# Kernel tuning notes

Hardware: AMD Instinct MI355X
Metric: run time of the kernel (lower is better)

## Reference

```python
import jax, jax.numpy as jnp
import numpy as np

N_NODES = 100000
N_EDGES = 100000
NNZ = 3200000
D_IN, D_HID, N_CLS = 512, 16, 7
NEG_SLOPE = 0.2


def _segment_softmax(scores, seg, num_segments, sorted_seg):
    m = jax.ops.segment_max(scores, seg, num_segments=num_segments,
                            indices_are_sorted=sorted_seg)
    ex = jnp.exp(scores - m[seg])
    s = jax.ops.segment_sum(ex, seg, num_segments=num_segments,
                            indices_are_sorted=sorted_seg)
    return ex / (s[seg] + 1e-9)


def _hypergat_layer(X, W, a1, a2, node_idx, edge_idx):
    # X: [N, din] -> h: [N, dout]
    h = X @ W
    hv = h[node_idx]                                   # [nnz, dout] gather
    # phase 1: node -> hyperedge attention (softmax within each hyperedge)
    s1 = jax.nn.leaky_relu(hv @ a1, NEG_SLOPE)         # [nnz]
    alpha = _segment_softmax(s1, edge_idx, N_EDGES, True)
    e = jax.ops.segment_sum(alpha[:, None] * hv, edge_idx,
                            num_segments=N_EDGES, indices_are_sorted=True)
    # phase 2: hyperedge -> node attention (softmax over edges incident to node)
    ev = e[edge_idx]                                   # [nnz, dout] gather
    s2 = jax.nn.leaky_relu(jnp.concatenate([hv, ev], axis=-1) @ a2, NEG_SLOPE)
    beta = _segment_softmax(s2, node_idx, N_NODES, False)
    out = jax.ops.segment_sum(beta[:, None] * ev, node_idx,
                              num_segments=N_NODES)
    return out


def setup_inputs() -> dict:
    key = jax.random.key(0)
    ks = jax.random.split(key, 8)
    H = jax.random.normal(ks[0], (N_NODES, D_IN), dtype=jnp.float32)
    node_idx = jax.random.randint(ks[1], (NNZ,), 0, N_NODES)
    edge_idx = jnp.sort(jax.random.randint(ks[2], (NNZ,), 0, N_EDGES))
    g1 = 1.0 / np.sqrt(D_IN)
    g2 = 1.0 / np.sqrt(D_HID)
    W1 = jax.random.uniform(ks[3], (D_IN, D_HID), jnp.float32, -g1, g1)
    a1_1 = jax.random.uniform(ks[4], (D_HID,), jnp.float32, -g2, g2)
    a2_1 = jax.random.uniform(ks[5], (2 * D_HID,), jnp.float32, -g2, g2)
    W2 = jax.random.uniform(ks[6], (D_HID, N_CLS), jnp.float32, -g2, g2)
    k7, k8 = jax.random.split(ks[7])
    gc = 1.0 / np.sqrt(N_CLS)
    a1_2 = jax.random.uniform(k7, (N_CLS,), jnp.float32, -gc, gc)
    a2_2 = jax.random.uniform(k8, (2 * N_CLS,), jnp.float32, -gc, gc)
    return {"H": H, "W1": W1, "a1_1": a1_1, "a2_1": a2_1,
            "W2": W2, "a1_2": a1_2, "a2_2": a2_2,
            "node_idx": node_idx, "edge_idx": edge_idx}


def reference(H, W1, a1_1, a2_1, W2, a1_2, a2_2, node_idx, edge_idx):
    H1 = _hypergat_layer(H, W1, a1_1, a2_1, node_idx, edge_idx)   # [N, 16]
    X2 = jax.nn.elu(H1)                                           # dropout off (eval)
    H2 = _hypergat_layer(X2, W2, a1_2, a2_2, node_idx, edge_idx)  # [N, 7]
    logp = jax.nn.log_softmax(H2, axis=1)
    return (logp, H1, H2)
```

## Files before the change

### kernel.cpp

```cpp
#include <hip/hip_runtime.h>
#include <hip/hip_bf16.h>
#include <math.h>

#define N_NODES 100000
#define N_EDGESC 100000
#define NNZ_C   3200000
#define D_IN    512
#define D_HID   16
#define N_CLS   7
#define NBK     782

typedef short short8 __attribute__((ext_vector_type(8)));
typedef float f32x4  __attribute__((ext_vector_type(4)));

__device__ __forceinline__ unsigned short f2bf_rn(float x) {
  unsigned int u = __float_as_uint(x);
  u += 0x7fff + ((u >> 16) & 1);
  return (unsigned short)(u >> 16);
}
__device__ __forceinline__ float bf2f(unsigned short b) {
  return __uint_as_float(((unsigned int)b) << 16);
}

__global__ void eoff_kernel(const int* __restrict__ eidx, int* __restrict__ eoff, int nnz, int E) {
  int i = blockIdx.x * blockDim.x + threadIdx.x;
  if (i >= nnz) return;
  int ec = eidx[i];
  int ep = (i == 0) ? -1 : eidx[i - 1];
  for (int e = ep + 1; e <= ec; ++e) eoff[e] = i;
  if (i == nnz - 1) {
    for (int e = ec + 1; e <= E; ++e) eoff[e] = nnz;
  }
}

__global__ void hist_kernel(const int* __restrict__ nidx, int* __restrict__ gcnt, int nnz) {
  __shared__ int lh[NBK];
  int t = threadIdx.x;
  for (int i = t; i < NBK; i += 256) lh[i] = 0;
  __syncthreads();
  int base = blockIdx.x * 12800;
  for (int it = 0; it < 50; ++it) {
    int i = base + it * 256 + t;
    if (i < nnz) atomicAdd(&lh[nidx[i] >> 7], 1);
  }
  __syncthreads();
  for (int i = t; i < NBK; i += 256) {
    int c = lh[i];
    if (c) atomicAdd(&gcnt[i], c);
  }
}

__global__ void bscan_kernel(const int* __restrict__ gcnt, int* __restrict__ boff,
                             int* __restrict__ bcur) {
  __shared__ int lds[1024];
  int t = threadIdx.x;
  int v = (t < NBK) ? gcnt[t] : 0;
  lds[t] = v;
  __syncthreads();
  for (int d = 1; d < 1024; d <<= 1) {
    int u = (t >= d) ? lds[t - d] : 0;
    __syncthreads();
    lds[t] += u;
    __syncthreads();
  }
  if (t < NBK) {
    boff[t + 1] = lds[t];
    bcur[t] = lds[t] - v;
  }
  if (t == 0) boff[0] = 0;
}

__global__ void bin_kernel(const int* __restrict__ nidx, const int* __restrict__ eidx,
                           int* __restrict__ bcur, int* __restrict__ binned, int nnz) {
  __shared__ int lh[NBK];
  __shared__ int gb[NBK];
  int t = threadIdx.x;
  for (int i = t; i < NBK; i += 256) lh[i] = 0;
  __syncthreads();
  int base = blockIdx.x * 12800;
  for (int it = 0; it < 50; ++it) {
    int i = base + it * 256 + t;
    if (i < nnz) atomicAdd(&lh[nidx[i] >> 7], 1);
  }
  __syncthreads();
  for (int i = t; i < NBK; i += 256) {
    int c = lh[i];
    gb[i] = c ? atomicAdd(&bcur[i], c) : 0;
    lh[i] = 0;
  }
  __syncthreads();
  for (int it = 0; it < 50; ++it) {
    int i = base + it * 256 + t;
    if (i < nnz) {
      int v = nidx[i], e = eidx[i];
      int bk = v >> 7;
      int r = atomicAdd(&lh[bk], 1);
      binned[gb[bk] + r] = e | ((v & 127) << 20);
    }
  }
}

__global__ void csr_kernel(const int* __restrict__ binned, const int* __restrict__ boff,
                           int* __restrict__ noff, int* __restrict__ perm_e, int N) {
  __shared__ int lh[128];
  __shared__ int lsc[128];
  __shared__ int lcur[128];
  int b = blockIdx.x;
  int t = threadIdx.x;
  int s = boff[b], e = boff[b + 1];
  if (t < 128) lh[t] = 0;
  __syncthreads();
  for (int i = s + t; i < e; i += 256) {
    atomicAdd(&lh[binned[i] >> 20], 1);
  }
  __syncthreads();
  if (t < 128) lsc[t] = lh[t];
  __syncthreads();
  for (int d = 1; d < 128; d <<= 1) {
    int u = (t < 128 && t >= d) ? lsc[t - d] : 0;
    __syncthreads();
    if (t < 128) lsc[t] += u;
    __syncthreads();
  }
  if (t < 128) {
    int excl = lsc[t] - lh[t];
    lcur[t] = excl;
    int n = b * 128 + t;
    if (n <= N) noff[n] = s + excl;
  }
  __syncthreads();
  for (int i = s + t; i < e; i += 256) {
    int p = binned[i];
    int r = atomicAdd(&lcur[p >> 20], 1);
    perm_e[s + r] = p & 0xFFFFF;
  }
}

__global__ __launch_bounds__(256) void gemm1_kernel(
    const float* __restrict__ X, const float* __restrict__ W,
    const float* __restrict__ a1, const float* __restrict__ a2,
    float* __restrict__ Hout, float2* __restrict__ phv, int numTiles) {
  int wid = blockIdx.x * 4 + (threadIdx.x >> 6);
  if (wid >= numTiles) return;
  int lane = threadIdx.x & 63;
  int col  = lane & 15;
  int quad = lane >> 4;

  short8 wh[16], wl[16];
#pragma unroll
  for (int c = 0; c < 16; ++c) {
#pragma unroll
    for (int j = 0; j < 8; ++j) {
      float w = W[(c * 32 + quad * 8 + j) * 16 + col];
      unsigned short h = f2bf_rn(w);
      wh[c][j] = (short)h;
      wl[c][j] = (short)f2bf_rn(w - bf2f(h));
    }
  }

  int rowbase = wid * 16;
  const float4* Xr = (const float4*)(X + (size_t)(rowbase + col) * D_IN) + quad * 2;

  f32x4 acc_hh = {0.f, 0.f, 0.f, 0.f};
  f32x4 acc_hl = {0.f, 0.f, 0.f, 0.f};
  f32x4 acc_lh = {0.f, 0.f, 0.f, 0.f};

  float4 u0 = Xr[0], u1 = Xr[1];
#pragma unroll
  for (int c = 0; c < 16; ++c) {
    float4 n0, n1;
    if (c < 15) { n0 = Xr[(c + 1) * 8]; n1 = Xr[(c + 1) * 8 + 1]; }
    float xs[8] = {u0.x, u0.y, u0.z, u0.w, u1.x, u1.y, u1.z, u1.w};
    short8 ah, al;
#pragma unroll
    for (int j = 0; j < 8; ++j) {
      unsigned short h = f2bf_rn(xs[j]);
      ah[j] = (short)h;
      al[j] = (short)f2bf_rn(xs[j] - bf2f(h));
    }
    acc_hh = __builtin_amdgcn_mfma_f32_16x16x32_bf16(ah, wh[c], acc_hh, 0, 0, 0);
    acc_hl = __builtin_amdgcn_mfma_f32_16x16x32_bf16(ah, wl[c], acc_hl, 0, 0, 0);
    acc_lh = __builtin_amdgcn_mfma_f32_16x16x32_bf16(al, wh[c], acc_lh, 0, 0, 0);
    u0 = n0; u1 = n1;
  }

  float a1c = a1[col], a2c = a2[col];
#pragma unroll
  for (int r = 0; r < 4; ++r) {
    float v = acc_hh[r] + acc_hl[r] + acc_lh[r];
    int row = rowbase + quad * 4 + r;
    Hout[(size_t)row * 16 + col] = v;
    float p1 = v * a1c, p2 = v * a2c;
#pragma unroll
    for (int d = 1; d < 16; d <<= 1) { p1 += __shfl_xor(p1, d); p2 += __shfl_xor(p2, d); }
    if (col == 0) phv[row] = make_float2(p1, p2);
  }
}

__global__ void gemm2_kernel(const float* __restrict__ H1, const float* __restrict__ W2,
                             const float* __restrict__ a1, const float* __restrict__ a2,
                             float* __restrict__ h2, float2* __restrict__ phv, int N) {
  __shared__ float w[D_HID * N_CLS];
  if (threadIdx.x < D_HID * N_CLS) w[threadIdx.x] = W2[threadIdx.x];
  __syncthreads();
  int v = blockIdx.x * blockDim.x + threadIdx.x;
  if (v >= N) return;
  const float4* h4 = (const float4*)(H1 + (size_t)v * D_HID);
  float x[16];
#pragma unroll
  for (int q = 0; q < 4; ++q) {
    float4 f = h4[q];
    x[q * 4 + 0] = f.x; x[q * 4 + 1] = f.y; x[q * 4 + 2] = f.z; x[q * 4 + 3] = f.w;
  }
#pragma unroll
  for (int k = 0; k < 16; ++k) x[k] = x[k] > 0.f ? x[k] : expm1f(x[k]);
  float p1 = 0.f, p2 = 0.f;
#pragma unroll
  for (int jj = 0; jj < N_CLS; ++jj) {
    float acc = 0.f;
#pragma unroll
    for (int k = 0; k < 16; ++k) acc += x[k] * w[k * N_CLS + jj];
    h2[(size_t)v * N_CLS + jj] = acc;
    p1 += acc * a1[jj];
    p2 += acc * a2[jj];
  }
  phv[v] = make_float2(p1, p2);
}

template <int D, int GROUP>
__global__ void edge_phase(const float* __restrict__ h, const float2* __restrict__ phv,
                           const float* __restrict__ a2,
                           const int* __restrict__ eoff, const int* __restrict__ nidx,
                           float* __restrict__ eout, float* __restrict__ pe, int E) {
  constexpr int NG = 64 / GROUP;
  int wave = (blockIdx.x * blockDim.x + threadIdx.x) >> 6;
  int lane = threadIdx.x & 63;
  if (wave >= E) return;
  int o0 = eoff[wave], o1 = eoff[wave + 1];
  int g = lane / GROUP, t = lane % GROUP;
  if (o0 == o1) {
    if (g == 0 && t < D) eout[(size_t)wave * D + t] = 0.f;
    if (lane == 0) pe[wave] = 0.f;
    return;
  }
  float m = -1e30f, l = 0.f;
  for (int i = o0 + lane; i < o1; i += 64) {
    float p = phv[nidx[i]].x;
    float s = p > 0.f ? p : 0.2f * p;
    float mn = fmaxf(m, s);
    l = l * __expf(m - mn) + __expf(s - mn);
    m = mn;
  }
#pragma unroll
  for (int d = 1; d < 64; d <<= 1) {
    float mo = __shfl_xor(m, d), lo = __shfl_xor(l, d);
    float mn = fmaxf(m, mo);
    l = l * __expf(m - mn) + lo * __expf(mo - mn);
    m = mn;
  }
  float acc = 0.f;
  for (int i = o0 + g; i < o1; i += NG) {
    int v = nidx[i];
    float p = phv[v].x;
    float s = p > 0.f ? p : 0.2f * p;
    float ex = __expf(s - m);
    float hv = (t < D) ? h[(size_t)v * D + t] : 0.f;
    acc += ex * hv;
  }
#pragma unroll
  for (int d = GROUP; d < 64; d <<= 1) acc += __shfl_xor(acc, d);
  float val = acc / (l + 1e-9f);
  float pa = (t < D) ? val * a2[D + t] : 0.f;
#pragma unroll
  for (int d = 1; d < GROUP; d <<= 1) pa += __shfl_xor(pa, d);
  if (g == 0) {
    if (t < D) eout[(size_t)wave * D + t] = val;
    if (t == 0) pe[wave] = pa;
  }
}

template <int D, int GROUP>
__global__ void node_phase(const float2* __restrict__ phv, const float* __restrict__ eoutv,
                           const float* __restrict__ pe, const int* __restrict__ noff,
                           const int* __restrict__ perm_e, float* __restrict__ out, int N) {
  constexpr int NG = 64 / GROUP;
  int wave = (blockIdx.x * blockDim.x + threadIdx.x) >> 6;
  int lane = threadIdx.x & 63;
  if (wave >= N) return;
  int o0 = noff[wave], o1 = noff[wave + 1];
  int g = lane / GROUP, t = lane % GROUP;
  if (o0 == o1) {
    if (g == 0 && t < D) out[(size_t)wave * D + t] = 0.f;
    return;
  }
  float ph = phv[wave].y;
  float m = -1e30f, l = 0.f;
  for (int i = o0 + lane; i < o1; i += 64) {
    float p = ph + pe[perm_e[i]];
    float s = p > 0.f ? p : 0.2f * p;
    float mn = fmaxf(m, s);
    l = l * __expf(m - mn) + __expf(s - mn);
    m = mn;
  }
#pragma unroll
  for (int d = 1; d < 64; d <<= 1) {
    float mo = __shfl_xor(m, d), lo = __shfl_xor(l, d);
    float mn = fmaxf(m, mo);
    l = l * __expf(m - mn) + lo * __expf(mo - mn);
    m = mn;
  }
  float acc = 0.f;
  for (int i = o0 + g; i < o1; i += NG) {
    int e = perm_e[i];
    float p = ph + pe[e];
    float s = p > 0.f ? p : 0.2f * p;
    float ex = __expf(s - m);
    float ev = (t < D) ? eoutv[(size_t)e * D + t] : 0.f;
    acc += ex * ev;
  }
#pragma unroll
  for (int d = GROUP; d < 64; d <<= 1) acc += __shfl_xor(acc, d);
  if (g == 0 && t < D) out[(size_t)wave * D + t] = acc / (l + 1e-9f);
}

__global__ void logsm_kernel(const float* __restrict__ H2, float* __restrict__ logp, int N) {
  int v = blockIdx.x * blockDim.x + threadIdx.x;
  if (v >= N) return;
  float x[N_CLS];
#pragma unroll
  for (int j = 0; j < N_CLS; ++j) x[j] = H2[(size_t)v * N_CLS + j];
  float m = x[0];
#pragma unroll
  for (int j = 1; j < N_CLS; ++j) m = fmaxf(m, x[j]);
  float s = 0.f;
#pragma unroll
  for (int j = 0; j < N_CLS; ++j) s += __expf(x[j] - m);
  float l = logf(s);
#pragma unroll
  for (int j = 0; j < N_CLS; ++j) logp[(size_t)v * N_CLS + j] = x[j] - m - l;
}


extern "C" void kernel_launch(void* const* d_in, const int* in_sizes, int n_in,
                              void* d_out, int out_size, void* d_ws, size_t ws_size,
                              hipStream_t stream) {
  const float* H    = (const float*)d_in[0];
  const float* W1   = (const float*)d_in[1];
  const float* a1_1 = (const float*)d_in[2];
  const float* a2_1 = (const float*)d_in[3];
  const float* W2   = (const float*)d_in[4];
  const float* a1_2 = (const float*)d_in[5];
  const float* a2_2 = (const float*)d_in[6];
  const int* nidx   = (const int*)d_in[7];
  const int* eidx   = (const int*)d_in[8];

  float* outp = (float*)d_out;
  float* logp = outp;
  float* H1   = outp + (size_t)N_NODES * N_CLS;
  float* H2   = H1 + (size_t)N_NODES * D_HID;

  char* ws = (char*)d_ws;
  int*   binned = (int*)(ws + 0);
  float* h1g  = (float*)(ws + 0);
  float* e1   = (float*)(ws + 6400000);
  float* h2g  = (float*)(ws + 12800000);
  float* e2   = (float*)(ws + 15600000);
  int* eoff   = (int*)(ws + 18400000);
  int* noff   = (int*)(ws + 18800128);
  float* pe   = (float*)(ws + 19200256);
  int* perm_e = (int*)(ws + 19600384);
  float2* phv = (float2*)(ws + 32400384);
  int* gcnt   = (int*)(ws + 33200384);
  int* boff   = (int*)(ws + 33203584);
  int* bcur   = (int*)(ws + 33206784);

  const int TB = 256;
  const int nnz_blocks = (NNZ_C + TB - 1) / TB;

  hipMemsetAsync(gcnt, 0, NBK * sizeof(int), stream);
  eoff_kernel<<<nnz_blocks, TB, 0, stream>>>(eidx, eoff, NNZ_C, N_EDGESC);
  hist_kernel<<<250, TB, 0, stream>>>(nidx, gcnt, NNZ_C);
  bscan_kernel<<<1, 1024, 0, stream>>>(gcnt, boff, bcur);
  bin_kernel<<<250, TB, 0, stream>>>(nidx, eidx, bcur, binned, NNZ_C);
  csr_kernel<<<NBK, TB, 0, stream>>>(binned, boff, noff, perm_e, N_NODES);

  {
    const int TILES = (N_NODES + 15) / 16;
    gemm1_kernel<<<(TILES + 3) / 4, TB, 0, stream>>>(H, W1, a1_1, a2_1, h1g, phv, TILES);
  }
  edge_phase<D_HID, 16><<<(N_EDGESC + 3) / 4, TB, 0, stream>>>(h1g, phv, a2_1, eoff, nidx, e1, pe, N_EDGESC);
  node_phase<D_HID, 16><<<(N_NODES + 3) / 4, TB, 0, stream>>>(phv, e1, pe, noff, perm_e, H1, N_NODES);

  gemm2_kernel<<<(N_NODES + TB - 1) / TB, TB, 0, stream>>>(H1, W2, a1_2, a2_2, h2g, phv, N_NODES);
  edge_phase<N_CLS, 8><<<(N_EDGESC + 3) / 4, TB, 0, stream>>>(h2g, phv, a2_2, eoff, nidx, e2, pe, N_EDGESC);
  node_phase<N_CLS, 8><<<(N_NODES + 3) / 4, TB, 0, stream>>>(phv, e2, pe, noff, perm_e, H2, N_NODES);

  logsm_kernel<<<(N_NODES + TB - 1) / TB, TB, 0, stream>>>(H2, logp, N_NODES);
}
```

Measured before the change: 743.4 us.

## Fuse preprocessing with GEMM/edge phases and use single-pass online softmax aggregation

```diff
diff --git a/kernel.cpp b/kernel.cpp
--- a/kernel.cpp
+++ b/kernel.cpp
@@ -10,6 +10,11 @@
 #define N_CLS   7
 #define NBK     782
 
+#define G_GEMM 1563
+#define G_EOFF 12500
+#define G_HIST 250
+#define G_BIN  250
+
 typedef short short8 __attribute__((ext_vector_type(8)));
 typedef float f32x4  __attribute__((ext_vector_type(4)));
 
@@ -22,31 +27,64 @@
   return __uint_as_float(((unsigned int)b) << 16);
 }
 
-__global__ void eoff_kernel(const int* __restrict__ eidx, int* __restrict__ eoff, int nnz, int E) {
-  int i = blockIdx.x * blockDim.x + threadIdx.x;
-  if (i >= nnz) return;
+__device__ __forceinline__ void eoff_body(int b, const int* __restrict__ eidx,
+                                          int* __restrict__ eoff) {
+  int i = b * 256 + threadIdx.x;
+  if (i >= NNZ_C) return;
   int ec = eidx[i];
   int ep = (i == 0) ? -1 : eidx[i - 1];
   for (int e = ep + 1; e <= ec; ++e) eoff[e] = i;
-  if (i == nnz - 1) {
-    for (int e = ec + 1; e <= E; ++e) eoff[e] = nnz;
-  }
-}
-
-__global__ void hist_kernel(const int* __restrict__ nidx, int* __restrict__ gcnt, int nnz) {
+  if (i == NNZ_C - 1) {
+    for (int e = ec + 1; e <= N_EDGESC; ++e) eoff[e] = NNZ_C;
+  }
+}
+
+__device__ __forceinline__ void hist_body(int b, const int* __restrict__ nidx,
+                                          int* __restrict__ gcnt) {
   __shared__ int lh[NBK];
   int t = threadIdx.x;
   for (int i = t; i < NBK; i += 256) lh[i] = 0;
   __syncthreads();
-  int base = blockIdx.x * 12800;
+  int base = b * 12800;
   for (int it = 0; it < 50; ++it) {
     int i = base + it * 256 + t;
-    if (i < nnz) atomicAdd(&lh[nidx[i] >> 7], 1);
+    if (i < NNZ_C) atomicAdd(&lh[nidx[i] >> 7], 1);
   }
   __syncthreads();
   for (int i = t; i < NBK; i += 256) {
     int c = lh[i];
     if (c) atomicAdd(&gcnt[i], c);
+  }
+}
+
+__device__ __forceinline__ void bin_body(int b, const int* __restrict__ nidx,
+                                         const int* __restrict__ eidx,
+                                         int* __restrict__ bcur, int* __restrict__ binned) {
+  __shared__ int lh[NBK];
+  __shared__ int gb[NBK];
+  int t = threadIdx.x;
+  for (int i = t; i < NBK; i += 256) lh[i] = 0;
+  __syncthreads();
+  int base = b * 12800;
+  for (int it = 0; it < 50; ++it) {
+    int i = base + it * 256 + t;
+    if (i < NNZ_C) atomicAdd(&lh[nidx[i] >> 7], 1);
+  }
+  __syncthreads();
+  for (int i = t; i < NBK; i += 256) {
+    int c = lh[i];
+    gb[i] = c ? atomicAdd(&bcur[i], c) : 0;
+    lh[i] = 0;
+  }
+  __syncthreads();
+  for (int it = 0; it < 50; ++it) {
+    int i = base + it * 256 + t;
+    if (i < NNZ_C) {
+      int v = nidx[i], e = eidx[i];
+      int bk = v >> 7;
+      int r = atomicAdd(&lh[bk], 1);
+      binned[gb[bk] + r] = e | ((v & 127) << 20);
+    }
   }
 }
 
@@ -68,36 +106,6 @@
     bcur[t] = lds[t] - v;
   }
   if (t == 0) boff[0] = 0;
-}
-
-__global__ void bin_kernel(const int* __restrict__ nidx, const int* __restrict__ eidx,
-                           int* __restrict__ bcur, int* __restrict__ binned, int nnz) {
-  __shared__ int lh[NBK];
-  __shared__ int gb[NBK];
-  int t = threadIdx.x;
-  for (int i = t; i < NBK; i += 256) lh[i] = 0;
-  __syncthreads();
-  int base = blockIdx.x * 12800;
-  for (int it = 0; it < 50; ++it) {
-    int i = base + it * 256 + t;
-    if (i < nnz) atomicAdd(&lh[nidx[i] >> 7], 1);
-  }
-  __syncthreads();
-  for (int i = t; i < NBK; i += 256) {
-    int c = lh[i];
-    gb[i] = c ? atomicAdd(&bcur[i], c) : 0;
-    lh[i] = 0;
-  }
-  __syncthreads();
-  for (int it = 0; it < 50; ++it) {
-    int i = base + it * 256 + t;
-    if (i < nnz) {
-      int v = nidx[i], e = eidx[i];
-      int bk = v >> 7;
-      int r = atomicAdd(&lh[bk], 1);
-      binned[gb[bk] + r] = e | ((v & 127) << 20);
-    }
-  }
 }
 
 __global__ void csr_kernel(const int* __restrict__ binned, const int* __restrict__ boff,
@@ -136,12 +144,12 @@
   }
 }
 
-__global__ __launch_bounds__(256) void gemm1_kernel(
+__device__ __forceinline__ void gemm1_body(int b,
     const float* __restrict__ X, const float* __restrict__ W,
     const float* __restrict__ a1, const float* __restrict__ a2,
-    float* __restrict__ Hout, float2* __restrict__ phv, int numTiles) {
-  int wid = blockIdx.x * 4 + (threadIdx.x >> 6);
-  if (wid >= numTiles) return;
+    float* __restrict__ Hout, float2* __restrict__ phv) {
+  int wid = b * 4 + (threadIdx.x >> 6);
+  if (wid >= 6250) return;
   int lane = threadIdx.x & 63;
   int col  = lane & 15;
   int quad = lane >> 4;
@@ -197,149 +205,215 @@
   }
 }
 
-__global__ void gemm2_kernel(const float* __restrict__ H1, const float* __restrict__ W2,
-                             const float* __restrict__ a1, const float* __restrict__ a2,
-                             float* __restrict__ h2, float2* __restrict__ phv, int N) {
-  __shared__ float w[D_HID * N_CLS];
-  if (threadIdx.x < D_HID * N_CLS) w[threadIdx.x] = W2[threadIdx.x];
-  __syncthreads();
-  int v = blockIdx.x * blockDim.x + threadIdx.x;
-  if (v >= N) return;
-  const float4* h4 = (const float4*)(H1 + (size_t)v * D_HID);
-  float x[16];
-#pragma unroll
-  for (int q = 0; q < 4; ++q) {
-    float4 f = h4[q];
-    x[q * 4 + 0] = f.x; x[q * 4 + 1] = f.y; x[q * 4 + 2] = f.z; x[q * 4 + 3] = f.w;
-  }
-#pragma unroll
-  for (int k = 0; k < 16; ++k) x[k] = x[k] > 0.f ? x[k] : expm1f(x[k]);
-  float p1 = 0.f, p2 = 0.f;
-#pragma unroll
-  for (int jj = 0; jj < N_CLS; ++jj) {
-    float acc = 0.f;
-#pragma unroll
-    for (int k = 0; k < 16; ++k) acc += x[k] * w[k * N_CLS + jj];
-    h2[(size_t)v * N_CLS + jj] = acc;
-    p1 += acc * a1[jj];
-    p2 += acc * a2[jj];
-  }
-  phv[v] = make_float2(p1, p2);
+__global__ __launch_bounds__(256) void k1_kernel(
+    const float* __restrict__ X, const float* __restrict__ W1,
+    const float* __restrict__ a1, const float* __restrict__ a2,
+    float* __restrict__ Hout, float2* __restrict__ phv,
+    const int* __restrict__ eidx, int* __restrict__ eoff,
+    const int* __restrict__ nidx, int* __restrict__ gcnt) {
+  int b = blockIdx.x;
+  if (b < G_GEMM) {
+    gemm1_body(b, X, W1, a1, a2, Hout, phv);
+  } else if (b < G_GEMM + G_EOFF) {
+    eoff_body(b - G_GEMM, eidx, eoff);
+  } else {
+    hist_body(b - G_GEMM - G_EOFF, nidx, gcnt);
+  }
 }
 
 template <int D, int GROUP>
-__global__ void edge_phase(const float* __restrict__ h, const float2* __restrict__ phv,
-                           const float* __restrict__ a2,
-                           const int* __restrict__ eoff, const int* __restrict__ nidx,
-                           float* __restrict__ eout, float* __restrict__ pe, int E) {
+__device__ __forceinline__ void edge_body(
+    const float* __restrict__ h, const float2* __restrict__ phv,
+    const float* __restrict__ a2, const int* __restrict__ eoff,
+    const int* __restrict__ nidx, float* __restrict__ eout,
+    float* __restrict__ pe, int E, int wave, int lane) {
   constexpr int NG = 64 / GROUP;
-  int wave = (blockIdx.x * blockDim.x + threadIdx.x) >> 6;
-  int lane = threadIdx.x & 63;
   if (wave >= E) return;
   int o0 = eoff[wave], o1 = eoff[wave + 1];
   int g = lane / GROUP, t = lane % GROUP;
   if (o0 == o1) {
-    if (g == 0 && t < D) eout[(size_t)wave * D + t] = 0.f;
-    if (lane == 0) pe[wave] = 0.f;
+    if (g == 0) {
+      if (t < D) eout[(size_t)wave * D + t] = 0.f;
+      if (t == 0) pe[wave] = 0.f;
+    }
     return;
   }
-  float m = -1e30f, l = 0.f;
-  for (int i = o0 + lane; i < o1; i += 64) {
-    float p = phv[nidx[i]].x;
-    float s = p > 0.f ? p : 0.2f * p;
-    float mn = fmaxf(m, s);
-    l = l * __expf(m - mn) + __expf(s - mn);
-    m = mn;
-  }
-#pragma unroll
-  for (int d = 1; d < 64; d <<= 1) {
-    float mo = __shfl_xor(m, d), lo = __shfl_xor(l, d);
+  float m = -1e30f, l = 0.f, acc = 0.f;
+  for (int i = o0 + g; i < o1; i += 2 * NG) {
+    int i2 = i + NG;
+    bool okb = i2 < o1;
+    int va = nidx[i];
+    int vb = okb ? nidx[i2] : va;
+    float pa_ = phv[va].x;
+    float pb_ = phv[vb].x;
+    float ha = (t < D) ? h[(size_t)va * D + t] : 0.f;
+    float hb = (t < D) ? h[(size_t)vb * D + t] : 0.f;
+    float sa = pa_ > 0.f ? pa_ : 0.2f * pa_;
+    float sb = pb_ > 0.f ? pb_ : 0.2f * pb_;
+    if (!okb) sb = -1e30f;
+    float mn = fmaxf(m, fmaxf(sa, sb));
+    float eo = __expf(m - mn);
+    float exa = __expf(sa - mn);
+    float exb = __expf(sb - mn);
+    l = l * eo + exa + exb;
+    acc = acc * eo + exa * ha + exb * hb;
+    m = mn;
+  }
+#pragma unroll
+  for (int d = GROUP; d < 64; d <<= 1) {
+    float mo = __shfl_xor(m, d), lo = __shfl_xor(l, d), ao = __shfl_xor(acc, d);
     float mn = fmaxf(m, mo);
-    l = l * __expf(m - mn) + lo * __expf(mo - mn);
-    m = mn;
-  }
-  float acc = 0.f;
-  for (int i = o0 + g; i < o1; i += NG) {
-    int v = nidx[i];
-    float p = phv[v].x;
-    float s = p > 0.f ? p : 0.2f * p;
-    float ex = __expf(s - m);
-    float hv = (t < D) ? h[(size_t)v * D + t] : 0.f;
-    acc += ex * hv;
-  }
-#pragma unroll
-  for (int d = GROUP; d < 64; d <<= 1) acc += __shfl_xor(acc, d);
+    float e0 = __expf(m - mn), e1x = __expf(mo - mn);
+    l = l * e0 + lo * e1x;
+    acc = acc * e0 + ao * e1x;
+    m = mn;
+  }
   float val = acc / (l + 1e-9f);
-  float pa = (t < D) ? val * a2[D + t] : 0.f;
-#pragma unroll
-  for (int d = 1; d < GROUP; d <<= 1) pa += __shfl_xor(pa, d);
+  float pav = (t < D) ? val * a2[D + t] : 0.f;
+#pragma unroll
+  for (int d = 1; d < GROUP; d <<= 1) pav += __shfl_xor(pav, d);
   if (g == 0) {
     if (t < D) eout[(size_t)wave * D + t] = val;
-    if (t == 0) pe[wave] = pa;
+    if (t == 0) pe[wave] = pav;
   }
 }
 
 template <int D, int GROUP>
-__global__ void node_phase(const float2* __restrict__ phv, const float* __restrict__ eoutv,
-                           const float* __restrict__ pe, const int* __restrict__ noff,
-                           const int* __restrict__ perm_e, float* __restrict__ out, int N) {
-  constexpr int NG = 64 / GROUP;
+__global__ void edge_kernel(const float* __restrict__ h, const float2* __restrict__ phv,
+                            const float* __restrict__ a2, const int* __restrict__ eoff,
+                            const int* __restrict__ nidx, float* __restrict__ eout,
+                            float* __restrict__ pe, int E) {
+  int wave = (blockIdx.x * blockDim.x + threadIdx.x) >> 6;
+  edge_body<D, GROUP>(h, phv, a2, eoff, nidx, eout, pe, E, wave, threadIdx.x & 63);
+}
+
+__global__ void k3_kernel(const int* __restrict__ nidx, const int* __restrict__ eidx,
+                          int* __restrict__ bcur, int* __restrict__ binned,
+                          const float* __restrict__ h1g, const float2* __restrict__ phv,
+                          const float* __restrict__ a2_1, const int* __restrict__ eoff,
+                          float* __restrict__ e1, float* __restrict__ pe) {
+  int b = blockIdx.x;
+  if (b < G_BIN) {
+    bin_body(b, nidx, eidx, bcur, binned);
+  } else {
+    int wave = (b - G_BIN) * 4 + (threadIdx.x >> 6);
+    edge_body<D_HID, 16>(h1g, phv, a2_1, eoff, nidx, e1, pe, N_EDGESC,
+                         wave, threadIdx.x & 63);
+  }
+}
+
+__global__ void node1_kernel(float2* phv, const float* __restrict__ e1,
+                             const float* __restrict__ pe, const int* __restrict__ noff,
+                             const int* __restrict__ perm_e, float* __restrict__ H1out,
+                             float* __restrict__ h2g, const float* __restrict__ W2,
+                             const float* __restrict__ a1_2, const float* __restrict__ a2_2,
+                             int N) {
   int wave = (blockIdx.x * blockDim.x + threadIdx.x) >> 6;
   int lane = threadIdx.x & 63;
   if (wave >= N) return;
   int o0 = noff[wave], o1 = noff[wave + 1];
-  int g = lane / GROUP, t = lane % GROUP;
-  if (o0 == o1) {
-    if (g == 0 && t < D) out[(size_t)wave * D + t] = 0.f;
-    return;
-  }
+  int g = lane >> 4, t = lane & 15;
   float ph = phv[wave].y;
-  float m = -1e30f, l = 0.f;
-  for (int i = o0 + lane; i < o1; i += 64) {
-    float p = ph + pe[perm_e[i]];
-    float s = p > 0.f ? p : 0.2f * p;
-    float mn = fmaxf(m, s);
-    l = l * __expf(m - mn) + __expf(s - mn);
-    m = mn;
-  }
-#pragma unroll
-  for (int d = 1; d < 64; d <<= 1) {
-    float mo = __shfl_xor(m, d), lo = __shfl_xor(l, d);
+  float m = -1e30f, l = 0.f, acc = 0.f;
+  for (int i = o0 + g; i < o1; i += 8) {
+    int i2 = i + 4;
+    bool okb = i2 < o1;
+    int ea = perm_e[i];
+    int eb = okb ? perm_e[i2] : ea;
+    float pa_ = ph + pe[ea];
+    float pb_ = ph + pe[eb];
+    float va = e1[(size_t)ea * 16 + t];
+    float vb = e1[(size_t)eb * 16 + t];
+    float sa = pa_ > 0.f ? pa_ : 0.2f * pa_;
+    float sb = pb_ > 0.f ? pb_ : 0.2f * pb_;
+    if (!okb) sb = -1e30f;
+    float mn = fmaxf(m, fmaxf(sa, sb));
+    float eo = __expf(m - mn);
+    float exa = __expf(sa - mn);
+    float exb = __expf(sb - mn);
+    l = l * eo + exa + exb;
+    acc = acc * eo + exa * va + exb * vb;
+    m = mn;
+  }
+#pragma unroll
+  for (int d = 16; d < 64; d <<= 1) {
+    float mo = __shfl_xor(m, d), lo = __shfl_xor(l, d), ao = __shfl_xor(acc, d);
     float mn = fmaxf(m, mo);
-    l = l * __expf(m - mn) + lo * __expf(mo - mn);
-    m = mn;
-  }
-  float acc = 0.f;
-  for (int i = o0 + g; i < o1; i += NG) {
-    int e = perm_e[i];
-    float p = ph + pe[e];
-    float s = p > 0.f ? p : 0.2f * p;
-    float ex = __expf(s - m);
-    float ev = (t < D) ? eoutv[(size_t)e * D + t] : 0.f;
-    acc += ex * ev;
-  }
-#pragma unroll
-  for (int d = GROUP; d < 64; d <<= 1) acc += __shfl_xor(acc, d);
-  if (g == 0 && t < D) out[(size_t)wave * D + t] = acc / (l + 1e-9f);
-}
-
-__global__ void logsm_kernel(const float* __restrict__ H2, float* __restrict__ logp, int N) {
-  int v = blockIdx.x * blockDim.x + threadIdx.x;
-  if (v >= N) return;
-  float x[N_CLS];
-#pragma unroll
-  for (int j = 0; j < N_CLS; ++j) x[j] = H2[(size_t)v * N_CLS + j];
-  float m = x[0];
-#pragma unroll
-  for (int j = 1; j < N_CLS; ++j) m = fmaxf(m, x[j]);
-  float s = 0.f;
-#pragma unroll
-  for (int j = 0; j < N_CLS; ++j) s += __expf(x[j] - m);
-  float l = logf(s);
-#pragma unroll
-  for (int j = 0; j < N_CLS; ++j) logp[(size_t)v * N_CLS + j] = x[j] - m - l;
-}
-
+    float e0 = __expf(m - mn), e1x = __expf(mo - mn);
+    l = l * e0 + lo * e1x;
+    acc = acc * e0 + ao * e1x;
+    m = mn;
+  }
+  float val = acc / (l + 1e-9f);
+  if (g == 0) H1out[(size_t)wave * 16 + t] = val;
+  float x = val > 0.f ? val : expm1f(val);
+  float p1 = 0.f, p2 = 0.f, myh2 = 0.f;
+#pragma unroll
+  for (int j = 0; j < N_CLS; ++j) {
+    float term = x * W2[t * N_CLS + j];
+#pragma unroll
+    for (int d = 1; d < 16; d <<= 1) term += __shfl_xor(term, d);
+    p1 += term * a1_2[j];
+    p2 += term * a2_2[j];
+    if (t == j) myh2 = term;
+  }
+  if (g == 0) {
+    if (t < N_CLS) h2g[(size_t)wave * N_CLS + t] = myh2;
+    if (t == 0) phv[wave] = make_float2(p1, p2);
+  }
+}
+
+__global__ void node2_kernel(const float2* __restrict__ phv, const float* __restrict__ e2,
+                             const float* __restrict__ pe, const int* __restrict__ noff,
+                             const int* __restrict__ perm_e, float* __restrict__ H2out,
+                             float* __restrict__ logp, int N) {
+  int wave = (blockIdx.x * blockDim.x + threadIdx.x) >> 6;
+  int lane = threadIdx.x & 63;
+  if (wave >= N) return;
+  int o0 = noff[wave], o1 = noff[wave + 1];
+  int g = lane >> 3, t = lane & 7;
+  float ph = phv[wave].y;
+  float m = -1e30f, l = 0.f, acc = 0.f;
+  for (int i = o0 + g; i < o1; i += 16) {
+    int i2 = i + 8;
+    bool okb = i2 < o1;
+    int ea = perm_e[i];
+    int eb = okb ? perm_e[i2] : ea;
+    float pa_ = ph + pe[ea];
+    float pb_ = ph + pe[eb];
+    float va = (t < N_CLS) ? e2[(size_t)ea * N_CLS + t] : 0.f;
+    float vb = (t < N_CLS) ? e2[(size_t)eb * N_CLS + t] : 0.f;
+    float sa = pa_ > 0.f ? pa_ : 0.2f * pa_;
+    float sb = pb_ > 0.f ? pb_ : 0.2f * pb_;
+    if (!okb) sb = -1e30f;
+    float mn = fmaxf(m, fmaxf(sa, sb));
+    float eo = __expf(m - mn);
+    float exa = __expf(sa - mn);
+    float exb = __expf(sb - mn);
+    l = l * eo + exa + exb;
+    acc = acc * eo + exa * va + exb * vb;
+    m = mn;
+  }
+#pragma unroll
+  for (int d = 8; d < 64; d <<= 1) {
+    float mo = __shfl_xor(m, d), lo = __shfl_xor(l, d), ao = __shfl_xor(acc, d);
+    float mn = fmaxf(m, mo);
+    float e0 = __expf(m - mn), e1x = __expf(mo - mn);
+    l = l * e0 + lo * e1x;
+    acc = acc * e0 + ao * e1x;
+    m = mn;
+  }
+  float val = acc / (l + 1e-9f);
+  if (g == 0 && t < N_CLS) H2out[(size_t)wave * N_CLS + t] = val;
+  float xm = (t < N_CLS) ? val : -1e30f;
+#pragma unroll
+  for (int d = 1; d < 8; d <<= 1) xm = fmaxf(xm, __shfl_xor(xm, d));
+  float se = (t < N_CLS) ? __expf(val - xm) : 0.f;
+#pragma unroll
+  for (int d = 1; d < 8; d <<= 1) se += __shfl_xor(se, d);
+  float lg = logf(se);
+  if (g == 0 && t < N_CLS) logp[(size_t)wave * N_CLS + t] = val - xm - lg;
+}
 
 extern "C" void kernel_launch(void* const* d_in, const int* in_sizes, int n_in,
                               void* d_out, int out_size, void* d_ws, size_t ws_size,
@@ -360,7 +434,6 @@
   float* H2   = H1 + (size_t)N_NODES * D_HID;
 
   char* ws = (char*)d_ws;
-  int*   binned = (int*)(ws + 0);
   float* h1g  = (float*)(ws + 0);
   float* e1   = (float*)(ws + 6400000);
   float* h2g  = (float*)(ws + 12800000);
@@ -373,27 +446,19 @@
   int* gcnt   = (int*)(ws + 33200384);
   int* boff   = (int*)(ws + 33203584);
   int* bcur   = (int*)(ws + 33206784);
+  int* binned = (int*)(ws + 33210368);
 
   const int TB = 256;
-  const int nnz_blocks = (NNZ_C + TB - 1) / TB;
 
   hipMemsetAsync(gcnt, 0, NBK * sizeof(int), stream);
-  eoff_kernel<<<nnz_blocks, TB, 0, stream>>>(eidx, eoff, NNZ_C, N_EDGESC);
-  hist_kernel<<<250, TB, 0, stream>>>(nidx, gcnt, NNZ_C);
+  k1_kernel<<<G_GEMM + G_EOFF + G_HIST, TB, 0, stream>>>(
+      H, W1, a1_1, a2_1, h1g, phv, eidx, eoff, nidx, gcnt);
   bscan_kernel<<<1, 1024, 0, stream>>>(gcnt, boff, bcur);
-  bin_kernel<<<250, TB, 0, stream>>>(nidx, eidx, bcur, binned, NNZ_C);
+  k3_kernel<<<G_BIN + 25000, TB, 0, stream>>>(
+      nidx, eidx, bcur, binned, h1g, phv, a2_1, eoff, e1, pe);
   csr_kernel<<<NBK, TB, 0, stream>>>(binned, boff, noff, perm_e, N_NODES);
-
-  {
-    const int TILES = (N_NODES + 15) / 16;
-    gemm1_kernel<<<(TILES + 3) / 4, TB, 0, stream>>>(H, W1, a1_1, a2_1, h1g, phv, TILES);
-  }
-  edge_phase<D_HID, 16><<<(N_EDGESC + 3) / 4, TB, 0, stream>>>(h1g, phv, a2_1, eoff, nidx, e1, pe, N_EDGESC);
-  node_phase<D_HID, 16><<<(N_NODES + 3) / 4, TB, 0, stream>>>(phv, e1, pe, noff, perm_e, H1, N_NODES);
-
-  gemm2_kernel<<<(N_NODES + TB - 1) / TB, TB, 0, stream>>>(H1, W2, a1_2, a2_2, h2g, phv, N_NODES);
-  edge_phase<N_CLS, 8><<<(N_EDGESC + 3) / 4, TB, 0, stream>>>(h2g, phv, a2_2, eoff, nidx, e2, pe, N_EDGESC);
-  node_phase<N_CLS, 8><<<(N_NODES + 3) / 4, TB, 0, stream>>>(phv, e2, pe, noff, perm_e, H2, N_NODES);
-
-  logsm_kernel<<<(N_NODES + TB - 1) / TB, TB, 0, stream>>>(H2, logp, N_NODES);
-}
+  node1_kernel<<<25000, TB, 0, stream>>>(phv, e1, pe, noff, perm_e, H1, h2g,
+                                         W2, a1_2, a2_2, N_NODES);
+  edge_kernel<N_CLS, 8><<<25000, TB, 0, stream>>>(h2g, phv, a2_2, eoff, nidx, e2, pe, N_EDGESC);
+  node2_kernel<<<25000, TB, 0, stream>>>(phv, e2, pe, noff, perm_e, H2, logp, N_NODES);
+}
```

New measurement: 660.8 us. -11.1%, faster.
